# Performance work log

Hardware: AMD Instinct MI355X
Metric: run time of the kernel (lower is better)

Reference implementation:

```python
import jax, jax.numpy as jnp
import numpy as np

N_NODES = 64
N_EDGES = N_NODES * (N_NODES - 1)  # 4032 (fully connected, no self-loops)
BATCH = 64
N_IN = 64
N_HID = 128
N_OUT = 16


def _linear_params(key, fan_in, fan_out):
    # mimic torch nn.Linear default init: U(-1/sqrt(fan_in), 1/sqrt(fan_in))
    kw, kb = jax.random.split(key)
    s = 1.0 / np.sqrt(fan_in)
    W = jax.random.uniform(kw, (fan_in, fan_out), minval=-s, maxval=s, dtype=jnp.float32)
    b = jax.random.uniform(kb, (fan_out,), minval=-s, maxval=s, dtype=jnp.float32)
    return W, b


def setup_inputs() -> dict:
    key = jax.random.key(0)
    ks = jax.random.split(key, 10)
    # one-hot relation matrices for fully-connected graph without self loops
    pairs = np.array([(i, j) for i in range(N_NODES) for j in range(N_NODES) if i != j])
    eye = np.eye(N_NODES, dtype=np.float32)
    rel_send = jnp.asarray(eye[pairs[:, 0]])  # [E, N]
    rel_rec = jnp.asarray(eye[pairs[:, 1]])   # [E, N]

    x = jax.random.normal(ks[0], (BATCH, N_NODES, N_IN), dtype=jnp.float32)

    w1a, b1a = _linear_params(ks[1], N_IN, N_HID)
    w1b, b1b = _linear_params(ks[2], N_HID, N_HID)
    w2a, b2a = _linear_params(ks[3], 2 * N_HID, N_HID)
    w2b, b2b = _linear_params(ks[4], N_HID, N_HID)
    w3a, b3a = _linear_params(ks[5], N_HID, N_HID)
    w3b, b3b = _linear_params(ks[6], N_HID, N_HID)
    w4a, b4a = _linear_params(ks[7], 3 * N_HID, N_HID)  # factor=True
    w4b, b4b = _linear_params(ks[8], N_HID, N_HID)
    wout, bout = _linear_params(ks[9], N_HID, N_OUT)

    return dict(x=x, rel_rec=rel_rec, rel_send=rel_send,
                w1a=w1a, b1a=b1a, w1b=w1b, b1b=b1b,
                w2a=w2a, b2a=b2a, w2b=w2b, b2b=b2b,
                w3a=w3a, b3a=b3a, w3b=w3b, b3b=b3b,
                w4a=w4a, b4a=b4a, w4b=w4b, b4b=b4b,
                wout=wout, bout=bout)


def _mlp(x, wa, ba, wb, bb):
    # Linear -> ReLU -> Linear
    return jax.nn.relu(x @ wa + ba) @ wb + bb


def reference(x, rel_rec, rel_send,
              w1a, b1a, w1b, b1b,
              w2a, b2a, w2b, b2b,
              w3a, b3a, w3b, b3b,
              w4a, b4a, w4b, b4b,
              wout, bout):
    def node2edge(h):
        receivers = jnp.einsum('en,bnh->beh', rel_rec, h)
        senders = jnp.einsum('en,bnh->beh', rel_send, h)
        return jnp.concatenate([senders, receivers], axis=-1)  # [B,E,2H]

    def edge2node(e):
        agg = jnp.einsum('en,beh->bnh', rel_rec, e)
        norm = rel_rec.sum(0)[None, :, None]  # [1,N,1]
        return agg / (norm + 1e-6)

    h = _mlp(x, w1a, b1a, w1b, b1b)            # [B,N,H]
    e = _mlp(node2edge(h), w2a, b2a, w2b, b2b)  # [B,E,H]
    x_skip = e
    # factor=True branch
    n = _mlp(edge2node(e), w3a, b3a, w3b, b3b)  # [B,N,H]
    e2 = node2edge(n)                           # [B,E,2H]
    e2 = jnp.concatenate([e2, x_skip], axis=2)  # [B,E,3H]
    e2 = _mlp(e2, w4a, b4a, w4b, b4b)           # [B,E,H]
    return e2 @ wout + bout                     # [B,E,n_out]
```

## Files before the change

kernel.cpp:

```cpp
#include <hip/hip_runtime.h>
#include <hip/hip_bf16.h>


#define DI __device__ __forceinline__

typedef short bf16x8 __attribute__((ext_vector_type(8)));
typedef float f32x4 __attribute__((ext_vector_type(4)));
typedef unsigned short u16;
typedef unsigned long long u64;

static constexpr int NN = 64, NE = 4032, H = 128;

DI u16 f2bf(float f) {
  union { float f; unsigned u; } v; v.f = f;
  unsigned u = v.u;
  return (u16)((u + 0x7fffu + ((u >> 16) & 1u)) >> 16);
}
DI unsigned pk2(float a, float b) {
  union { __hip_bfloat162 h; unsigned u; } c;
  c.h = __float22bfloat162_rn(float2{a, b});
  return c.u;
}
DI f32x4 mf(bf16x8 a, bf16x8 b, f32x4 c) {
  return __builtin_amdgcn_mfma_f32_16x16x32_bf16(a, b, c, 0, 0, 0);
}
DI bf16x8 ldfrag(const u16* __restrict__ p, int idx, int l) {
  return *reinterpret_cast<const bf16x8*>(p + (idx * 64 + l) * 8);
}

__global__ __launch_bounds__(64) void prepack_kernel(
    const float* __restrict__ w1a, const float* __restrict__ w1b,
    const float* __restrict__ w2a, const float* __restrict__ w2b,
    const float* __restrict__ w3a, const float* __restrict__ w3b,
    const float* __restrict__ w4a, const float* __restrict__ w4b,
    const float* __restrict__ wout,
    const float* __restrict__ b2b, const float* __restrict__ b4b,
    const float* __restrict__ bout,
    u16* __restrict__ pk, float* __restrict__ c2, float* __restrict__ c4) {
  int seg = blockIdx.y, f = blockIdx.x, l = threadIdx.x;
  int h = l >> 4, mm = l & 15;
  if (seg == 10) {
    if (f >= 4) return;
    union { u16 u[8]; uint4 q; } o;
#pragma unroll
    for (int jj = 0; jj < 8; jj++) {
      int row = f * 32 + h * 8 + jj;
      float s0 = 0.f, s1 = 0.f, s2 = 0.f, s3 = 0.f;
      for (int j = 0; j < 128; j += 4) {
        s0 += w4b[row * 128 + j]     * wout[j * 16 + mm];
        s1 += w4b[row * 128 + j + 1] * wout[(j + 1) * 16 + mm];
        s2 += w4b[row * 128 + j + 2] * wout[(j + 2) * 16 + mm];
        s3 += w4b[row * 128 + j + 3] * wout[(j + 3) * 16 + mm];
      }
      o.u[jj] = f2bf((s0 + s1) + (s2 + s3));
    }
    *reinterpret_cast<uint4*>(pk + ((304 + f) * 64 + l) * 8) = o.q;
    return;
  }
  if (seg == 11) {
    if (f < 2) {
      int o = f * 64 + l;
      float s0 = 0.f, s1 = 0.f;
      for (int k = 0; k < 128; k += 2) {
        s0 += b2b[k] * w4a[(256 + k) * 128 + o];
        s1 += b2b[k + 1] * w4a[(256 + k + 1) * 128 + o];
      }
      c2[o] = s0 + s1;
    } else if (f == 2 && l < 16) {
      float s = bout[l];
      for (int k = 0; k < 128; k++) s += b4b[k] * wout[k * 16 + l];
      c4[l] = s;
    }
    return;
  }
  const float* src; int foff, nfrag, roff, pi;
  switch (seg) {
    case 0:  src = w1a; foff = 0;   nfrag = 16; roff = 0;   pi = 0; break;
    case 1:  src = w1b; foff = 16;  nfrag = 32; roff = 0;   pi = 1; break;
    case 2:  src = w2a; foff = 48;  nfrag = 32; roff = 0;   pi = 1; break;
    case 3:  src = w2a; foff = 80;  nfrag = 32; roff = 128; pi = 1; break;
    case 4:  src = w2b; foff = 112; nfrag = 32; roff = 0;   pi = 0; break;
    case 5:  src = w3a; foff = 144; nfrag = 32; roff = 0;   pi = 1; break;
    case 6:  src = w3b; foff = 176; nfrag = 32; roff = 0;   pi = 1; break;
    case 7:  src = w4a; foff = 208; nfrag = 32; roff = 0;   pi = 1; break;
    case 8:  src = w4a; foff = 240; nfrag = 32; roff = 128; pi = 1; break;
    default: src = w4a; foff = 272; nfrag = 32; roff = 256; pi = 0; break;
  }
  if (f >= nfrag) return;
  int kt = f >> 3, ct = f & 7;
  union { u16 u[8]; uint4 q; } o;
#pragma unroll
  for (int jj = 0; jj < 8; jj++) {
    int row = pi ? (kt * 32 + (jj >> 2) * 16 + h * 4 + (jj & 3))
                 : (kt * 32 + h * 8 + jj);
    o.u[jj] = f2bf(src[(roff + row) * 128 + ct * 16 + mm]);
  }
  *reinterpret_cast<uint4*>(pk + ((foff + f) * 64 + l) * 8) = o.q;
}

__global__ __launch_bounds__(512, 2) void node_kernel(
    const float* __restrict__ x, const u16* __restrict__ pk,
    const float* __restrict__ b1a, const float* __restrict__ b1b,
    const float* __restrict__ b2a,
    float* __restrict__ sproj, float* __restrict__ rproj) {
  __shared__ bf16x8 act[2][4][64];
  int blk = blockIdx.x, b = blk >> 2, nq = blk & 3;
  int tid = threadIdx.x, l = tid & 63, w = tid >> 6;
  int m = l & 15, h = l >> 4;
  int node = nq * 16 + m;
  const f32x4 Z = {0.f, 0.f, 0.f, 0.f};
  f32x4 acc;
  {
    const float* xb = x + (b * NN + node) * 64;
    bf16x8 xin[2];
#pragma unroll
    for (int kt = 0; kt < 2; kt++) {
      f32x4 a0 = *(const f32x4*)(xb + kt * 32 + h * 8);
      f32x4 a1 = *(const f32x4*)(xb + kt * 32 + h * 8 + 4);
      union { unsigned u[4]; bf16x8 v; } t;
      t.u[0] = pk2(a0[0], a0[1]); t.u[1] = pk2(a0[2], a0[3]);
      t.u[2] = pk2(a1[0], a1[1]); t.u[3] = pk2(a1[2], a1[3]);
      xin[kt] = t.v;
    }
    acc = mf(ldfrag(pk, w, l), xin[0], Z);
    acc = mf(ldfrag(pk, 8 + w, l), xin[1], acc);
    f32x4 bb = *(const f32x4*)(b1a + w * 16 + h * 4);
    union { unsigned u[2]; u64 d; } p;
    p.u[0] = pk2(fmaxf(acc[0] + bb[0], 0.f), fmaxf(acc[1] + bb[1], 0.f));
    p.u[1] = pk2(fmaxf(acc[2] + bb[2], 0.f), fmaxf(acc[3] + bb[3], 0.f));
    reinterpret_cast<u64*>(&act[0][w >> 1][l])[w & 1] = p.d;
  }
  __syncthreads();
  bf16x8 ef[4];
#pragma unroll
  for (int kt = 0; kt < 4; kt++) ef[kt] = act[0][kt][l];
#pragma unroll
  for (int kt = 0; kt < 4; kt++)
    acc = mf(ldfrag(pk + 16 * 512, kt * 8 + w, l), ef[kt], kt == 0 ? Z : acc);
  {
    f32x4 bb = *(const f32x4*)(b1b + w * 16 + h * 4);
    union { unsigned u[2]; u64 d; } p;
    p.u[0] = pk2(acc[0] + bb[0], acc[1] + bb[1]);
    p.u[1] = pk2(acc[2] + bb[2], acc[3] + bb[3]);
    reinterpret_cast<u64*>(&act[1][w >> 1][l])[w & 1] = p.d;
  }
  __syncthreads();
#pragma unroll
  for (int kt = 0; kt < 4; kt++) ef[kt] = act[1][kt][l];
#pragma unroll
  for (int kt = 0; kt < 4; kt++)
    acc = mf(ldfrag(pk + 48 * 512, kt * 8 + w, l), ef[kt], kt == 0 ? Z : acc);
  *reinterpret_cast<f32x4*>(sproj + (b * NN + node) * H + w * 16 + h * 4) = acc;
#pragma unroll
  for (int kt = 0; kt < 4; kt++)
    acc = mf(ldfrag(pk + 80 * 512, kt * 8 + w, l), ef[kt], kt == 0 ? Z : acc);
  {
    f32x4 bb = *(const f32x4*)(b2a + w * 16 + h * 4);
    f32x4 o = acc;
    o[0] += bb[0]; o[1] += bb[1]; o[2] += bb[2]; o[3] += bb[3];
    *reinterpret_cast<f32x4*>(rproj + (b * NN + node) * H + w * 16 + h * 4) = o;
  }
}

__global__ __launch_bounds__(512, 2) void agg_kernel(
    const float* __restrict__ sproj, const float* __restrict__ rproj,
    const u16* __restrict__ pk,
    const float* __restrict__ b2b, const float* __restrict__ b3a,
    const float* __restrict__ b3b, const float* __restrict__ b4a,
    const float* __restrict__ c2,
    float* __restrict__ s4, float* __restrict__ r4) {
  __shared__ f32x4 lred[8][8][64];
  __shared__ bf16x8 act[2][4][64];
  int blk = blockIdx.x, b = blk >> 2, jq = blk & 3;
  int tid = threadIdx.x, l = tid & 63, w = tid >> 6, m = l & 15, h = l >> 4;
  int j = jq * 16 + m;
  const float* rpb = rproj + (b * NN + j) * H;
  f32x4 rpv[8], accS[8];
#pragma unroll
  for (int k = 0; k < 8; k++) {
    rpv[k] = *(const f32x4*)(rpb + (k >> 1) * 32 + h * 8 + (k & 1) * 4);
    accS[k] = f32x4{0.f, 0.f, 0.f, 0.f};
  }
  const float* spb = sproj + b * NN * H;
  for (int i = w * 8; i < w * 8 + 8; i++) {
    const float* sp = spb + i * H;
#pragma unroll
    for (int k = 0; k < 8; k++) {
      f32x4 s = *(const f32x4*)(sp + (k >> 1) * 32 + h * 8 + (k & 1) * 4);
      f32x4 t = s + rpv[k];
      t[0] = fmaxf(t[0], 0.f); t[1] = fmaxf(t[1], 0.f);
      t[2] = fmaxf(t[2], 0.f); t[3] = fmaxf(t[3], 0.f);
      accS[k] += t;
    }
  }
  if ((j >> 3) == w) {
    const float* sp = spb + j * H;
#pragma unroll
    for (int k = 0; k < 8; k++) {
      f32x4 s = *(const f32x4*)(sp + (k >> 1) * 32 + h * 8 + (k & 1) * 4);
      f32x4 t = s + rpv[k];
      accS[k][0] -= fmaxf(t[0], 0.f); accS[k][1] -= fmaxf(t[1], 0.f);
      accS[k][2] -= fmaxf(t[2], 0.f); accS[k][3] -= fmaxf(t[3], 0.f);
    }
  }
#pragma unroll
  for (int k = 0; k < 8; k++) lred[w][k][l] = accS[k];
  __syncthreads();
  if (w < 4) {
    f32x4 s0 = f32x4{0.f, 0.f, 0.f, 0.f}, s1 = s0;
#pragma unroll
    for (int ww = 0; ww < 8; ww++) {
      s0 += lred[ww][2 * w][l];
      s1 += lred[ww][2 * w + 1][l];
    }
    union { unsigned u[4]; bf16x8 v; } t;
    t.u[0] = pk2(s0[0], s0[1]); t.u[1] = pk2(s0[2], s0[3]);
    t.u[2] = pk2(s1[0], s1[1]); t.u[3] = pk2(s1[2], s1[3]);
    act[0][w][l] = t.v;
  }
  __syncthreads();
  const f32x4 Z = {0.f, 0.f, 0.f, 0.f};
  f32x4 acc;
  bf16x8 ef[4];
#pragma unroll
  for (int kt = 0; kt < 4; kt++) ef[kt] = act[0][kt][l];
#pragma unroll
  for (int kt = 0; kt < 4; kt++)
    acc = mf(ldfrag(pk + 112 * 512, kt * 8 + w, l), ef[kt], kt == 0 ? Z : acc);
  {
    const float inv = 1.0f / (63.0f + 1e-6f);
    const float binv = 63.0f * inv;
    f32x4 bb = *(const f32x4*)(b2b + w * 16 + h * 4);
    union { unsigned u[2]; u64 d; } p;
    p.u[0] = pk2(acc[0] * inv + bb[0] * binv, acc[1] * inv + bb[1] * binv);
    p.u[1] = pk2(acc[2] * inv + bb[2] * binv, acc[3] * inv + bb[3] * binv);
    reinterpret_cast<u64*>(&act[1][w >> 1][l])[w & 1] = p.d;
  }
  __syncthreads();
#pragma unroll
  for (int kt = 0; kt < 4; kt++) ef[kt] = act[1][kt][l];
#pragma unroll
  for (int kt = 0; kt < 4; kt++)
    acc = mf(ldfrag(pk + 144 * 512, kt * 8 + w, l), ef[kt], kt == 0 ? Z : acc);
  {
    f32x4 bb = *(const f32x4*)(b3a + w * 16 + h * 4);
    union { unsigned u[2]; u64 d; } p;
    p.u[0] = pk2(fmaxf(acc[0] + bb[0], 0.f), fmaxf(acc[1] + bb[1], 0.f));
    p.u[1] = pk2(fmaxf(acc[2] + bb[2], 0.f), fmaxf(acc[3] + bb[3], 0.f));
    reinterpret_cast<u64*>(&act[0][w >> 1][l])[w & 1] = p.d;
  }
  __syncthreads();
#pragma unroll
  for (int kt = 0; kt < 4; kt++) ef[kt] = act[0][kt][l];
#pragma unroll
  for (int kt = 0; kt < 4; kt++)
    acc = mf(ldfrag(pk + 176 * 512, kt * 8 + w, l), ef[kt], kt == 0 ? Z : acc);
  {
    f32x4 bb = *(const f32x4*)(b3b + w * 16 + h * 4);
    union { unsigned u[2]; u64 d; } p;
    p.u[0] = pk2(acc[0] + bb[0], acc[1] + bb[1]);
    p.u[1] = pk2(acc[2] + bb[2], acc[3] + bb[3]);
    reinterpret_cast<u64*>(&act[1][w >> 1][l])[w & 1] = p.d;
  }
  __syncthreads();
#pragma unroll
  for (int kt = 0; kt < 4; kt++) ef[kt] = act[1][kt][l];
#pragma unroll
  for (int kt = 0; kt < 4; kt++)
    acc = mf(ldfrag(pk + 208 * 512, kt * 8 + w, l), ef[kt], kt == 0 ? Z : acc);
  {
    f32x4 cc = *(const f32x4*)(c2 + w * 16 + h * 4);
    f32x4 o = acc;
    o[0] += cc[0]; o[1] += cc[1]; o[2] += cc[2]; o[3] += cc[3];
    *reinterpret_cast<f32x4*>(s4 + (b * NN + j) * H + w * 16 + h * 4) = o;
  }
#pragma unroll
  for (int kt = 0; kt < 4; kt++)
    acc = mf(ldfrag(pk + 240 * 512, kt * 8 + w, l), ef[kt], kt == 0 ? Z : acc);
  {
    f32x4 bb = *(const f32x4*)(b4a + w * 16 + h * 4);
    f32x4 o = acc;
    o[0] += bb[0]; o[1] += bb[1]; o[2] += bb[2]; o[3] += bb[3];
    *reinterpret_cast<f32x4*>(r4 + (b * NN + j) * H + w * 16 + h * 4) = o;
  }
}

__global__ __launch_bounds__(256, 4) void edge_kernel(
    const float* __restrict__ sproj, const float* __restrict__ rproj,
    const float* __restrict__ s4, const float* __restrict__ r4,
    const u16* __restrict__ pk, const float* __restrict__ c4,
    float* __restrict__ out) {
  __shared__ alignas(16) u16 bufA[8192];
  __shared__ alignas(16) u16 bufB[8192];
  int blk = blockIdx.x;
  int wg = (blk & 7) * 512 + (blk >> 3);
  int b = wg >> 6, i = wg & 63;
  int tid = threadIdx.x, l = tid & 63, w = tid >> 6;
  int m16 = l & 15, h = l >> 4;
  const f32x4 Z = {0.f, 0.f, 0.f, 0.f};
  int jnv[4];
#pragma unroll
  for (int n = 0; n < 4; n++) {
    int e = n * 16 + m16;
    int v = e + (e >= i ? 1 : 0); jnv[n] = v > 63 ? 63 : v;
  }
  {
    const float* spp = sproj + (b * NN + i) * H + w * 32 + h * 8;
    f32x4 s0 = *(const f32x4*)spp, s1 = *(const f32x4*)(spp + 4);
#pragma unroll
    for (int n = 0; n < 4; n++) {
      const float* rpp = rproj + (b * NN + jnv[n]) * H + w * 32 + h * 8;
      f32x4 r0 = *(const f32x4*)rpp, r1 = *(const f32x4*)(rpp + 4);
      union { unsigned u[4]; uint4 q; } t;
      t.u[0] = pk2(fmaxf(s0[0] + r0[0], 0.f), fmaxf(s0[1] + r0[1], 0.f));
      t.u[1] = pk2(fmaxf(s0[2] + r0[2], 0.f), fmaxf(s0[3] + r0[3], 0.f));
      t.u[2] = pk2(fmaxf(s1[0] + r1[0], 0.f), fmaxf(s1[1] + r1[1], 0.f));
      t.u[3] = pk2(fmaxf(s1[2] + r1[2], 0.f), fmaxf(s1[3] + r1[3], 0.f));
      *reinterpret_cast<uint4*>(&bufA[((w * 4 + n) * 64 + l) * 8]) = t.q;
    }
  }
  bf16x8 wv[8];
#pragma unroll
  for (int idx = 0; idx < 8; idx++)
    wv[idx] = ldfrag(pk + 112 * 512, (idx >> 1) * 8 + 2 * w + (idx & 1), l);
  __syncthreads();
  f32x4 acc[2][4];
  __builtin_amdgcn_s_setprio(1);
#pragma unroll
  for (int n = 0; n < 4; n++) {
    bf16x8 bf[4];
#pragma unroll
    for (int kt = 0; kt < 4; kt++)
      bf[kt] = *reinterpret_cast<const bf16x8*>(&bufA[((kt * 4 + n) * 64 + l) * 8]);
#pragma unroll
    for (int kt = 0; kt < 4; kt++)
#pragma unroll
      for (int m = 0; m < 2; m++)
        acc[m][n] = mf(wv[kt * 2 + m], bf[kt], kt == 0 ? Z : acc[m][n]);
  }
  __builtin_amdgcn_s_setprio(0);
#pragma unroll
  for (int idx = 0; idx < 8; idx++)
    wv[idx] = ldfrag(pk + 272 * 512, (idx >> 1) * 8 + 2 * w + (idx & 1), l);
  {
    int lane2b = (h >> 1) * 16 + m16;
    int jb = (h & 1) * 4;
#pragma unroll
    for (int m = 0; m < 2; m++)
#pragma unroll
      for (int n = 0; n < 4; n++) {
        union { unsigned u[2]; u64 d; } p;
        p.u[0] = pk2(acc[m][n][0], acc[m][n][1]);
        p.u[1] = pk2(acc[m][n][2], acc[m][n][3]);
        *reinterpret_cast<u64*>(
            &bufB[((w * 4 + n) * 64 + lane2b + m * 32) * 8 + jb]) = p.d;
      }
  }
  f32x4 s4v[2], rv[4][2];
#pragma unroll
  for (int m = 0; m < 2; m++)
    s4v[m] = *(const f32x4*)(s4 + (b * NN + i) * H + w * 32 + m * 16 + h * 4);
#pragma unroll
  for (int n = 0; n < 4; n++) {
    const float* r4p = r4 + (b * NN + jnv[n]) * H + w * 32 + h * 4;
#pragma unroll
    for (int m = 0; m < 2; m++) rv[n][m] = *(const f32x4*)(r4p + m * 16);
  }
  __syncthreads();
  __builtin_amdgcn_s_setprio(1);
#pragma unroll
  for (int n = 0; n < 4; n++) {
    bf16x8 bf[4];
#pragma unroll
    for (int kt = 0; kt < 4; kt++)
      bf[kt] = *reinterpret_cast<const bf16x8*>(&bufB[((kt * 4 + n) * 64 + l) * 8]);
#pragma unroll
    for (int kt = 0; kt < 4; kt++)
#pragma unroll
      for (int m = 0; m < 2; m++)
        acc[m][n] = mf(wv[kt * 2 + m], bf[kt], kt == 0 ? Z : acc[m][n]);
  }
  __builtin_amdgcn_s_setprio(0);
  {
    int lane2b = (h >> 1) * 16 + m16;
    int jb = (h & 1) * 4;
#pragma unroll
    for (int n = 0; n < 4; n++)
#pragma unroll
      for (int m = 0; m < 2; m++) {
        f32x4 r = rv[n][m];
        union { unsigned u[2]; u64 d; } p;
        p.u[0] = pk2(fmaxf(acc[m][n][0] + s4v[m][0] + r[0], 0.f),
                     fmaxf(acc[m][n][1] + s4v[m][1] + r[1], 0.f));
        p.u[1] = pk2(fmaxf(acc[m][n][2] + s4v[m][2] + r[2], 0.f),
                     fmaxf(acc[m][n][3] + s4v[m][3] + r[3], 0.f));
        *reinterpret_cast<u64*>(
            &bufA[((w * 4 + n) * 64 + lane2b + m * 32) * 8 + jb]) = p.d;
      }
  }
  __syncthreads();
  {
    bf16x8 wfv[4], bf[4];
#pragma unroll
    for (int kt = 0; kt < 4; kt++) {
      wfv[kt] = ldfrag(pk + 304 * 512, kt, l);
      bf[kt] = *reinterpret_cast<const bf16x8*>(&bufA[((kt * 4 + w) * 64 + l) * 8]);
    }
    f32x4 a4 = Z;
#pragma unroll
    for (int kt = 0; kt < 4; kt++) a4 = mf(wfv[kt], bf[kt], a4);
    int jj = w * 16 + m16;
    if (jj < 63) {
      f32x4 c4v = *(const f32x4*)(c4 + h * 4);
      f32x4 o;
      o[0] = a4[0] + c4v[0]; o[1] = a4[1] + c4v[1];
      o[2] = a4[2] + c4v[2]; o[3] = a4[3] + c4v[3];
      *reinterpret_cast<f32x4*>(out + (b * NE + i * 63 + jj) * 16 + h * 4) = o;
    }
  }
}

extern "C" void kernel_launch(void* const* d_in, const int* in_sizes, int n_in,
                              void* d_out, int out_size, void* d_ws, size_t ws_size,
                              hipStream_t stream) {
  const float* x    = (const float*)d_in[0];
  const float* w1a  = (const float*)d_in[3];
  const float* b1a  = (const float*)d_in[4];
  const float* w1b  = (const float*)d_in[5];
  const float* b1b  = (const float*)d_in[6];
  const float* w2a  = (const float*)d_in[7];
  const float* b2a  = (const float*)d_in[8];
  const float* w2b  = (const float*)d_in[9];
  const float* b2b  = (const float*)d_in[10];
  const float* w3a  = (const float*)d_in[11];
  const float* b3a  = (const float*)d_in[12];
  const float* w3b  = (const float*)d_in[13];
  const float* b3b  = (const float*)d_in[14];
  const float* w4a  = (const float*)d_in[15];
  const float* b4a  = (const float*)d_in[16];
  const float* w4b  = (const float*)d_in[17];
  const float* b4b  = (const float*)d_in[18];
  const float* wout = (const float*)d_in[19];
  const float* bout = (const float*)d_in[20];
  float* out = (float*)d_out;

  float* sproj = (float*)d_ws;
  float* rproj = sproj + 524288;
  float* s4    = rproj + 524288;
  float* r4    = s4 + 524288;
  u16* pkw     = (u16*)(r4 + 524288);
  float* c2    = (float*)(pkw + 174080);
  float* c4    = c2 + 128;

  prepack_kernel<<<dim3(32, 12), 64, 0, stream>>>(
      w1a, w1b, w2a, w2b, w3a, w3b, w4a, w4b, wout, b2b, b4b, bout, pkw, c2, c4);
  node_kernel<<<256, 512, 0, stream>>>(x, pkw, b1a, b1b, b2a, sproj, rproj);
  agg_kernel<<<256, 512, 0, stream>>>(sproj, rproj, pkw, b2b, b3a, b3b, b4a, c2, s4, r4);
  edge_kernel<<<4096, 256, 0, stream>>>(sproj, rproj, s4, r4, pkw, c4, out);
}
```

Before: 84.68 us.

## Process two sender nodes per edge-kernel block to reuse weight fragments

Each edge_kernel block now handles two sender nodes (128 edges) instead of one, halving the grid to 2048 blocks. Weight fragments are loaded once per k-tile and applied to both node chunks, so each weight load is amortised over twice the MFMA work. The two LDS buffers are merged into one 32 KB buffer, with extra barriers between phases. The trade is more accumulator registers (acc doubles), which may lower occupancy under launch_bounds(256,4), and fewer blocks to spread across CUs.

```diff
diff --git a/kernel.cpp b/kernel.cpp
--- a/kernel.cpp
+++ b/kernel.cpp
@@ -290,132 +290,142 @@
     const float* __restrict__ s4, const float* __restrict__ r4,
     const u16* __restrict__ pk, const float* __restrict__ c4,
     float* __restrict__ out) {
-  __shared__ alignas(16) u16 bufA[8192];
-  __shared__ alignas(16) u16 bufB[8192];
+  __shared__ alignas(16) u16 buf[32 * 512];
   int blk = blockIdx.x;
-  int wg = (blk & 7) * 512 + (blk >> 3);
-  int b = wg >> 6, i = wg & 63;
+  int wg = (blk & 7) * 256 + (blk >> 3);
+  int b = wg >> 5, ip = wg & 31;
   int tid = threadIdx.x, l = tid & 63, w = tid >> 6;
   int m16 = l & 15, h = l >> 4;
   const f32x4 Z = {0.f, 0.f, 0.f, 0.f};
-  int jnv[4];
-#pragma unroll
-  for (int n = 0; n < 4; n++) {
-    int e = n * 16 + m16;
-    int v = e + (e >= i ? 1 : 0); jnv[n] = v > 63 ? 63 : v;
-  }
-  {
-    const float* spp = sproj + (b * NN + i) * H + w * 32 + h * 8;
+  int jnv[2][4];
+#pragma unroll
+  for (int ch = 0; ch < 2; ch++) {
+    int i = ip * 2 + ch;
+#pragma unroll
+    for (int n = 0; n < 4; n++) {
+      int e = n * 16 + m16;
+      int v = e + (e >= i ? 1 : 0); jnv[ch][n] = v > 63 ? 63 : v;
+    }
+  }
+#pragma unroll
+  for (int ch = 0; ch < 2; ch++) {
+    const float* spp = sproj + (b * NN + ip * 2 + ch) * H + w * 32 + h * 8;
     f32x4 s0 = *(const f32x4*)spp, s1 = *(const f32x4*)(spp + 4);
 #pragma unroll
     for (int n = 0; n < 4; n++) {
-      const float* rpp = rproj + (b * NN + jnv[n]) * H + w * 32 + h * 8;
+      const float* rpp = rproj + (b * NN + jnv[ch][n]) * H + w * 32 + h * 8;
       f32x4 r0 = *(const f32x4*)rpp, r1 = *(const f32x4*)(rpp + 4);
       union { unsigned u[4]; uint4 q; } t;
       t.u[0] = pk2(fmaxf(s0[0] + r0[0], 0.f), fmaxf(s0[1] + r0[1], 0.f));
       t.u[1] = pk2(fmaxf(s0[2] + r0[2], 0.f), fmaxf(s0[3] + r0[3], 0.f));
       t.u[2] = pk2(fmaxf(s1[0] + r1[0], 0.f), fmaxf(s1[1] + r1[1], 0.f));
       t.u[3] = pk2(fmaxf(s1[2] + r1[2], 0.f), fmaxf(s1[3] + r1[3], 0.f));
-      *reinterpret_cast<uint4*>(&bufA[((w * 4 + n) * 64 + l) * 8]) = t.q;
-    }
-  }
-  bf16x8 wv[8];
-#pragma unroll
-  for (int idx = 0; idx < 8; idx++)
-    wv[idx] = ldfrag(pk + 112 * 512, (idx >> 1) * 8 + 2 * w + (idx & 1), l);
-  __syncthreads();
-  f32x4 acc[2][4];
+      *reinterpret_cast<uint4*>(&buf[((ch * 16 + w * 4 + n) * 64 + l) * 8]) = t.q;
+    }
+  }
+  __syncthreads();
+  f32x4 acc[2][2][4];
   __builtin_amdgcn_s_setprio(1);
 #pragma unroll
-  for (int n = 0; n < 4; n++) {
-    bf16x8 bf[4];
-#pragma unroll
-    for (int kt = 0; kt < 4; kt++)
-      bf[kt] = *reinterpret_cast<const bf16x8*>(&bufA[((kt * 4 + n) * 64 + l) * 8]);
-#pragma unroll
-    for (int kt = 0; kt < 4; kt++)
-#pragma unroll
-      for (int m = 0; m < 2; m++)
-        acc[m][n] = mf(wv[kt * 2 + m], bf[kt], kt == 0 ? Z : acc[m][n]);
+  for (int kt = 0; kt < 4; kt++) {
+    bf16x8 wv0 = ldfrag(pk + 112 * 512, kt * 8 + 2 * w, l);
+    bf16x8 wv1 = ldfrag(pk + 112 * 512, kt * 8 + 2 * w + 1, l);
+#pragma unroll
+    for (int ch = 0; ch < 2; ch++)
+#pragma unroll
+      for (int n = 0; n < 4; n++) {
+        bf16x8 bf = *reinterpret_cast<const bf16x8*>(
+            &buf[((ch * 16 + kt * 4 + n) * 64 + l) * 8]);
+        acc[ch][0][n] = mf(wv0, bf, kt == 0 ? Z : acc[ch][0][n]);
+        acc[ch][1][n] = mf(wv1, bf, kt == 0 ? Z : acc[ch][1][n]);
+      }
   }
   __builtin_amdgcn_s_setprio(0);
-#pragma unroll
-  for (int idx = 0; idx < 8; idx++)
-    wv[idx] = ldfrag(pk + 272 * 512, (idx >> 1) * 8 + 2 * w + (idx & 1), l);
+  __syncthreads();
   {
     int lane2b = (h >> 1) * 16 + m16;
     int jb = (h & 1) * 4;
 #pragma unroll
-    for (int m = 0; m < 2; m++)
+    for (int ch = 0; ch < 2; ch++)
+#pragma unroll
+      for (int m = 0; m < 2; m++)
+#pragma unroll
+        for (int n = 0; n < 4; n++) {
+          union { unsigned u[2]; u64 d; } p;
+          p.u[0] = pk2(acc[ch][m][n][0], acc[ch][m][n][1]);
+          p.u[1] = pk2(acc[ch][m][n][2], acc[ch][m][n][3]);
+          *reinterpret_cast<u64*>(
+              &buf[((ch * 16 + w * 4 + n) * 64 + lane2b + m * 32) * 8 + jb]) = p.d;
+        }
+  }
+  __syncthreads();
+  __builtin_amdgcn_s_setprio(1);
+#pragma unroll
+  for (int kt = 0; kt < 4; kt++) {
+    bf16x8 wv0 = ldfrag(pk + 272 * 512, kt * 8 + 2 * w, l);
+    bf16x8 wv1 = ldfrag(pk + 272 * 512, kt * 8 + 2 * w + 1, l);
+#pragma unroll
+    for (int ch = 0; ch < 2; ch++)
 #pragma unroll
       for (int n = 0; n < 4; n++) {
-        union { unsigned u[2]; u64 d; } p;
-        p.u[0] = pk2(acc[m][n][0], acc[m][n][1]);
-        p.u[1] = pk2(acc[m][n][2], acc[m][n][3]);
-        *reinterpret_cast<u64*>(
-            &bufB[((w * 4 + n) * 64 + lane2b + m * 32) * 8 + jb]) = p.d;
-      }
-  }
-  f32x4 s4v[2], rv[4][2];
-#pragma unroll
-  for (int m = 0; m < 2; m++)
-    s4v[m] = *(const f32x4*)(s4 + (b * NN + i) * H + w * 32 + m * 16 + h * 4);
-#pragma unroll
-  for (int n = 0; n < 4; n++) {
-    const float* r4p = r4 + (b * NN + jnv[n]) * H + w * 32 + h * 4;
-#pragma unroll
-    for (int m = 0; m < 2; m++) rv[n][m] = *(const f32x4*)(r4p + m * 16);
-  }
-  __syncthreads();
-  __builtin_amdgcn_s_setprio(1);
-#pragma unroll
-  for (int n = 0; n < 4; n++) {
-    bf16x8 bf[4];
-#pragma unroll
-    for (int kt = 0; kt < 4; kt++)
-      bf[kt] = *reinterpret_cast<const bf16x8*>(&bufB[((kt * 4 + n) * 64 + l) * 8]);
-#pragma unroll
-    for (int kt = 0; kt < 4; kt++)
-#pragma unroll
-      for (int m = 0; m < 2; m++)
-        acc[m][n] = mf(wv[kt * 2 + m], bf[kt], kt == 0 ? Z : acc[m][n]);
+        bf16x8 bf = *reinterpret_cast<const bf16x8*>(
+            &buf[((ch * 16 + kt * 4 + n) * 64 + l) * 8]);
+        acc[ch][0][n] = mf(wv0, bf, kt == 0 ? Z : acc[ch][0][n]);
+        acc[ch][1][n] = mf(wv1, bf, kt == 0 ? Z : acc[ch][1][n]);
+      }
   }
   __builtin_amdgcn_s_setprio(0);
+  __syncthreads();
   {
     int lane2b = (h >> 1) * 16 + m16;
     int jb = (h & 1) * 4;
 #pragma unroll
-    for (int n = 0; n < 4; n++)
-#pragma unroll
-      for (int m = 0; m < 2; m++) {
-        f32x4 r = rv[n][m];
-        union { unsigned u[2]; u64 d; } p;
-        p.u[0] = pk2(fmaxf(acc[m][n][0] + s4v[m][0] + r[0], 0.f),
-                     fmaxf(acc[m][n][1] + s4v[m][1] + r[1], 0.f));
-        p.u[1] = pk2(fmaxf(acc[m][n][2] + s4v[m][2] + r[2], 0.f),
-                     fmaxf(acc[m][n][3] + s4v[m][3] + r[3], 0.f));
+    for (int ch = 0; ch < 2; ch++) {
+      const float* s4p = s4 + (b * NN + ip * 2 + ch) * H + w * 32 + h * 4;
+      f32x4 sA = *(const f32x4*)s4p;
+      f32x4 sB = *(const f32x4*)(s4p + 16);
+#pragma unroll
+      for (int n = 0; n < 4; n++) {
+        const float* r4p = r4 + (b * NN + jnv[ch][n]) * H + w * 32 + h * 4;
+        f32x4 rA = *(const f32x4*)r4p;
+        f32x4 rB = *(const f32x4*)(r4p + 16);
+        union { unsigned u[2]; u64 d; } pA, pB;
+        pA.u[0] = pk2(fmaxf(acc[ch][0][n][0] + sA[0] + rA[0], 0.f),
+                      fmaxf(acc[ch][0][n][1] + sA[1] + rA[1], 0.f));
+        pA.u[1] = pk2(fmaxf(acc[ch][0][n][2] + sA[2] + rA[2], 0.f),
+                      fmaxf(acc[ch][0][n][3] + sA[3] + rA[3], 0.f));
+        pB.u[0] = pk2(fmaxf(acc[ch][1][n][0] + sB[0] + rB[0], 0.f),
+                      fmaxf(acc[ch][1][n][1] + sB[1] + rB[1], 0.f));
+        pB.u[1] = pk2(fmaxf(acc[ch][1][n][2] + sB[2] + rB[2], 0.f),
+                      fmaxf(acc[ch][1][n][3] + sB[3] + rB[3], 0.f));
         *reinterpret_cast<u64*>(
-            &bufA[((w * 4 + n) * 64 + lane2b + m * 32) * 8 + jb]) = p.d;
-      }
-  }
-  __syncthreads();
-  {
-    bf16x8 wfv[4], bf[4];
-#pragma unroll
-    for (int kt = 0; kt < 4; kt++) {
-      wfv[kt] = ldfrag(pk + 304 * 512, kt, l);
-      bf[kt] = *reinterpret_cast<const bf16x8*>(&bufA[((kt * 4 + w) * 64 + l) * 8]);
-    }
-    f32x4 a4 = Z;
-#pragma unroll
-    for (int kt = 0; kt < 4; kt++) a4 = mf(wfv[kt], bf[kt], a4);
-    int jj = w * 16 + m16;
-    if (jj < 63) {
-      f32x4 c4v = *(const f32x4*)(c4 + h * 4);
-      f32x4 o;
-      o[0] = a4[0] + c4v[0]; o[1] = a4[1] + c4v[1];
-      o[2] = a4[2] + c4v[2]; o[3] = a4[3] + c4v[3];
-      *reinterpret_cast<f32x4*>(out + (b * NE + i * 63 + jj) * 16 + h * 4) = o;
+            &buf[((ch * 16 + w * 4 + n) * 64 + lane2b) * 8 + jb]) = pA.d;
+        *reinterpret_cast<u64*>(
+            &buf[((ch * 16 + w * 4 + n) * 64 + lane2b + 32) * 8 + jb]) = pB.d;
+      }
+    }
+  }
+  __syncthreads();
+  {
+    f32x4 c4v = *(const f32x4*)(c4 + h * 4);
+#pragma unroll
+    for (int ch = 0; ch < 2; ch++) {
+      f32x4 a4 = Z;
+#pragma unroll
+      for (int kt = 0; kt < 4; kt++) {
+        bf16x8 wfv = ldfrag(pk + 304 * 512, kt, l);
+        bf16x8 bf = *reinterpret_cast<const bf16x8*>(
+            &buf[((ch * 16 + kt * 4 + w) * 64 + l) * 8]);
+        a4 = mf(wfv, bf, a4);
+      }
+      int jj = w * 16 + m16;
+      if (jj < 63) {
+        int i = ip * 2 + ch;
+        f32x4 o;
+        o[0] = a4[0] + c4v[0]; o[1] = a4[1] + c4v[1];
+        o[2] = a4[2] + c4v[2]; o[3] = a4[3] + c4v[3];
+        *reinterpret_cast<f32x4*>(out + (b * NE + i * 63 + jj) * 16 + h * 4) = o;
+      }
     }
   }
 }
@@ -456,5 +466,5 @@
       w1a, w1b, w2a, w2b, w3a, w3b, w4a, w4b, wout, b2b, b4b, bout, pkw, c2, c4);
   node_kernel<<<256, 512, 0, stream>>>(x, pkw, b1a, b1b, b2a, sproj, rproj);
   agg_kernel<<<256, 512, 0, stream>>>(sproj, rproj, pkw, b2b, b3a, b3b, b4a, c2, s4, r4);
-  edge_kernel<<<4096, 256, 0, stream>>>(sproj, rproj, s4, r4, pkw, c4, out);
-}
+  edge_kernel<<<2048, 256, 0, stream>>>(sproj, rproj, s4, r4, pkw, c4, out);
+}
```

Result: slower. 86.68 us (+2.4%).
